# Kernel optimization log

Measured on AMD Instinct MI355X. Metric: run time of the kernel, lower is better.

The kernel has to match this reference:

```python
import jax, jax.numpy as jnp
import numpy as np

B, N, F = 512, 2048, 64
T = 4            # number of atom types
H1, H2 = 64, 32  # hidden widths; final layer outputs 1 (per-atom energy)


def setup_inputs() -> dict:
    key = jax.random.key(0)
    ks = jax.random.split(key, 8)
    x = jax.random.normal(ks[0], (B, N, F), dtype=jnp.float32)
    atomic_numbers = jax.random.randint(ks[1], (N,), 0, T)
    s = 0.05
    # Per-type MLP parameters, stacked over the type axis (torch Linear layout: [out, in]).
    w0 = jax.random.normal(ks[2], (T, H1, F), dtype=jnp.float32) * s
    b0 = jax.random.normal(ks[3], (T, H1), dtype=jnp.float32) * s
    w1 = jax.random.normal(ks[4], (T, H2, H1), dtype=jnp.float32) * s
    b1 = jax.random.normal(ks[5], (T, H2), dtype=jnp.float32) * s
    w2 = jax.random.normal(ks[6], (T, 1, H2), dtype=jnp.float32) * s
    b2 = jax.random.normal(ks[7], (T, 1), dtype=jnp.float32) * s
    return {"x": x, "atomic_numbers": atomic_numbers,
            "w0": w0, "b0": b0, "w1": w1, "b1": b1, "w2": w2, "b2": b2}


def reference(x, atomic_numbers, w0, b0, w1, b1, w2, b2):
    # Behler-Parrinello: route each atom through the MLP of its atom type,
    # then sum per-atom energies over atoms.  The torch version gathers atoms
    # by type, runs each type's MLP, and scatters back; here we evaluate all
    # T type-MLPs batched over the type axis and select with a one-hot mask
    # (identical math, jit-friendly, no data-dependent shapes).
    onehot = jax.nn.one_hot(atomic_numbers, w0.shape[0], dtype=x.dtype)  # [N, T]
    h = jax.nn.silu(jnp.einsum('bnf,thf->tbnh', x, w0) + b0[:, None, None, :])   # [T,B,N,H1]
    h = jax.nn.silu(jnp.einsum('tbnh,tgh->tbng', h, w1) + b1[:, None, None, :])  # [T,B,N,H2]
    e = jnp.einsum('tbng,tog->tbno', h, w2) + b2[:, None, None, :]               # [T,B,N,1]
    e = e[..., 0]                                                                # [T,B,N]
    per_atom = jnp.einsum('tbn,nt->bn', e, onehot)  # select the matching type per atom
    return per_atom.sum(axis=-1)                    # [B]
```

## Files before the change

### kernel.cpp

```cpp
#include <hip/hip_runtime.h>
#include <hip/hip_bf16.h>


#define B_ 512
#define N_ 2048
#define F_ 64
#define T_ 4
#define H1_ 64
#define H2_ 32

#define BT 16
#define NCHUNK 16

typedef __attribute__((ext_vector_type(8))) short bf16x8;
typedef __attribute__((ext_vector_type(4))) short bf16x4;
typedef __attribute__((ext_vector_type(4))) float f32x4;

__device__ inline float silu_f(float v) {
    return v * __builtin_amdgcn_rcpf(1.0f + __expf(-v));
}

__device__ inline bf16x8 pack8(float4 a, float4 b) {
    union { __hip_bfloat162 h[4]; bf16x8 v; } u;
    u.h[0] = __float22bfloat162_rn({a.x, a.y});
    u.h[1] = __float22bfloat162_rn({a.z, a.w});
    u.h[2] = __float22bfloat162_rn({b.x, b.y});
    u.h[3] = __float22bfloat162_rn({b.z, b.w});
    return u.v;
}

__device__ inline bf16x4 pack4(float a, float b, float c, float d) {
    union { __hip_bfloat162 h[2]; bf16x4 v; } u;
    u.h[0] = __float22bfloat162_rn({a, b});
    u.h[1] = __float22bfloat162_rn({c, d});
    return u.v;
}

__device__ inline float bf_at(bf16x4 v, int r) {
    union { bf16x4 v; __hip_bfloat16 h[4]; } u; u.v = v;
    return __bfloat162float(u.h[r]);
}

__global__ void sort_atoms(const int* __restrict__ an, int* __restrict__ sorted,
                           float* __restrict__ out) {
    const int lane = threadIdx.x;
#pragma unroll
    for (int i = 0; i < B_ / 64; ++i) out[i * 64 + lane] = 0.0f;

    int v[32];
#pragma unroll
    for (int c = 0; c < 32; ++c) v[c] = an[c * 64 + lane];

    int c0 = 0, c1 = 0, c2 = 0;
#pragma unroll
    for (int c = 0; c < 32; ++c) {
        c0 += __popcll(__ballot(v[c] == 0));
        c1 += __popcll(__ballot(v[c] == 1));
        c2 += __popcll(__ballot(v[c] == 2));
    }
    int base0 = 0, base1 = c0, base2 = c0 + c1, base3 = c0 + c1 + c2;
    const unsigned long long mb = (1ull << lane) - 1ull;
#pragma unroll
    for (int c = 0; c < 32; ++c) {
        const int t = v[c];
        unsigned long long m0 = __ballot(t == 0);
        unsigned long long m1 = __ballot(t == 1);
        unsigned long long m2 = __ballot(t == 2);
        unsigned long long m3 = __ballot(t == 3);
        int pos;
        if (t == 0)      pos = base0 + (int)__popcll(m0 & mb);
        else if (t == 1) pos = base1 + (int)__popcll(m1 & mb);
        else if (t == 2) pos = base2 + (int)__popcll(m2 & mb);
        else             pos = base3 + (int)__popcll(m3 & mb);
        sorted[pos] = (t << 16) | (c * 64 + lane);
        base0 += (int)__popcll(m0); base1 += (int)__popcll(m1);
        base2 += (int)__popcll(m2); base3 += (int)__popcll(m3);
    }
}

__global__ __launch_bounds__(64, 3) void bpnn_kernel(
    const float* __restrict__ x, const int* __restrict__ sorted,
    const float* __restrict__ w0, const float* __restrict__ b0,
    const float* __restrict__ w1, const float* __restrict__ b1,
    const float* __restrict__ w2, const float* __restrict__ b2,
    float* __restrict__ out)
{
    __shared__ __align__(16) __hip_bfloat16 trb[BT][68];

    const int lane = threadIdx.x;
    const int lr   = lane & 15;
    const int q    = lane >> 4;
    const int b0i  = blockIdx.y * BT;
    const int s0   = blockIdx.x * NCHUNK;

    int myid = 0;
    if (lane < NCHUNK) myid = sorted[s0 + lane];

    const float* xb_ = x + (size_t)(b0i + lr) * (N_ * F_) + q * 8;
    __hip_bfloat16* trbw = &trb[lr][0];

    float esum0 = 0.f, esum1 = 0.f, bsum = 0.f;

    bf16x8 aw000, aw001, aw010, aw011, aw020, aw021, aw030, aw031;
    bf16x8 aw100, aw101, aw110, aw111;
    bf16x4 b0f0, b0f1, b0f2, b0f3, b1f0, b1f1, w2f0, w2f1;
    float b2c = 0.f;

    int i = 0;
    int id0 = __builtin_amdgcn_readlane(myid, 0);
    int id1 = __builtin_amdgcn_readlane(myid, 1);
    float4 sa0, sa1, sa2, sa3, sb0, sb1, sb2, sb3;
    {
        const float4* pA = reinterpret_cast<const float4*>(xb_ + (size_t)(id0 & 0xFFFF) * F_);
        sa0 = pA[0]; sa1 = pA[1]; sa2 = pA[8]; sa3 = pA[9];
        const float4* pB = reinterpret_cast<const float4*>(xb_ + (size_t)(id1 & 0xFFFF) * F_);
        sb0 = pB[0]; sb1 = pB[1]; sb2 = pB[8]; sb3 = pB[9];
    }

    while (i < NCHUNK) {
        const int t = id0 >> 16;
        {
            const float* wb = w0 + t * (H1_ * F_) + lr * F_ + q * 8;
            const float4* pw;
            pw = reinterpret_cast<const float4*>(wb +  0 * F_ +  0); aw000 = pack8(pw[0], pw[1]);
            pw = reinterpret_cast<const float4*>(wb +  0 * F_ + 32); aw001 = pack8(pw[0], pw[1]);
            pw = reinterpret_cast<const float4*>(wb + 16 * F_ +  0); aw010 = pack8(pw[0], pw[1]);
            pw = reinterpret_cast<const float4*>(wb + 16 * F_ + 32); aw011 = pack8(pw[0], pw[1]);
            pw = reinterpret_cast<const float4*>(wb + 32 * F_ +  0); aw020 = pack8(pw[0], pw[1]);
            pw = reinterpret_cast<const float4*>(wb + 32 * F_ + 32); aw021 = pack8(pw[0], pw[1]);
            pw = reinterpret_cast<const float4*>(wb + 48 * F_ +  0); aw030 = pack8(pw[0], pw[1]);
            pw = reinterpret_cast<const float4*>(wb + 48 * F_ + 32); aw031 = pack8(pw[0], pw[1]);
            const float* wc = w1 + t * (H2_ * H1_) + lr * H1_ + q * 8;
            pw = reinterpret_cast<const float4*>(wc +  0 * H1_ +  0); aw100 = pack8(pw[0], pw[1]);
            pw = reinterpret_cast<const float4*>(wc +  0 * H1_ + 32); aw101 = pack8(pw[0], pw[1]);
            pw = reinterpret_cast<const float4*>(wc + 16 * H1_ +  0); aw110 = pack8(pw[0], pw[1]);
            pw = reinterpret_cast<const float4*>(wc + 16 * H1_ + 32); aw111 = pack8(pw[0], pw[1]);
            float4 v;
            v = *reinterpret_cast<const float4*>(b0 + t * H1_ +  0 + q * 4); b0f0 = pack4(v.x, v.y, v.z, v.w);
            v = *reinterpret_cast<const float4*>(b0 + t * H1_ + 16 + q * 4); b0f1 = pack4(v.x, v.y, v.z, v.w);
            v = *reinterpret_cast<const float4*>(b0 + t * H1_ + 32 + q * 4); b0f2 = pack4(v.x, v.y, v.z, v.w);
            v = *reinterpret_cast<const float4*>(b0 + t * H1_ + 48 + q * 4); b0f3 = pack4(v.x, v.y, v.z, v.w);
            v = *reinterpret_cast<const float4*>(b1 + t * H2_ +  0 + q * 4); b1f0 = pack4(v.x, v.y, v.z, v.w);
            v = *reinterpret_cast<const float4*>(b1 + t * H2_ + 16 + q * 4); b1f1 = pack4(v.x, v.y, v.z, v.w);
            v = *reinterpret_cast<const float4*>(w2 + t * H2_ +  0 + q * 4); w2f0 = pack4(v.x, v.y, v.z, v.w);
            v = *reinterpret_cast<const float4*>(w2 + t * H2_ + 16 + q * 4); w2f1 = pack4(v.x, v.y, v.z, v.w);
            b2c = b2[t];
        }

        for (;;) {
            bf16x8 xf0 = pack8(sa0, sa1);
            bf16x8 xf1 = pack8(sa2, sa3);
            sa0 = sb0; sa1 = sb1; sa2 = sb2; sa3 = sb3;
            int in2 = (i + 2 < NCHUNK) ? i + 2 : NCHUNK - 1;
            int idn = __builtin_amdgcn_readlane(myid, in2);
            {
                const float4* pB = reinterpret_cast<const float4*>(xb_ + (size_t)(idn & 0xFFFF) * F_);
                sb0 = pB[0]; sb1 = pB[1]; sb2 = pB[8]; sb3 = pB[9];
            }
            bsum += b2c;

            f32x4 acc0 = {0.f,0.f,0.f,0.f}, acc1 = {0.f,0.f,0.f,0.f};
            f32x4 acc2 = {0.f,0.f,0.f,0.f}, acc3 = {0.f,0.f,0.f,0.f};
            acc0 = __builtin_amdgcn_mfma_f32_16x16x32_bf16(aw000, xf0, acc0, 0, 0, 0);
            acc0 = __builtin_amdgcn_mfma_f32_16x16x32_bf16(aw001, xf1, acc0, 0, 0, 0);
            acc1 = __builtin_amdgcn_mfma_f32_16x16x32_bf16(aw010, xf0, acc1, 0, 0, 0);
            acc1 = __builtin_amdgcn_mfma_f32_16x16x32_bf16(aw011, xf1, acc1, 0, 0, 0);
            acc2 = __builtin_amdgcn_mfma_f32_16x16x32_bf16(aw020, xf0, acc2, 0, 0, 0);
            acc2 = __builtin_amdgcn_mfma_f32_16x16x32_bf16(aw021, xf1, acc2, 0, 0, 0);
            acc3 = __builtin_amdgcn_mfma_f32_16x16x32_bf16(aw030, xf0, acc3, 0, 0, 0);
            acc3 = __builtin_amdgcn_mfma_f32_16x16x32_bf16(aw031, xf1, acc3, 0, 0, 0);

            {
                float v0 = silu_f(acc0[0] + bf_at(b0f0, 0));
                float v1 = silu_f(acc0[1] + bf_at(b0f0, 1));
                float v2 = silu_f(acc0[2] + bf_at(b0f0, 2));
                float v3 = silu_f(acc0[3] + bf_at(b0f0, 3));
                *reinterpret_cast<bf16x4*>(trbw +  0 + q * 4) = pack4(v0, v1, v2, v3);
                v0 = silu_f(acc1[0] + bf_at(b0f1, 0));
                v1 = silu_f(acc1[1] + bf_at(b0f1, 1));
                v2 = silu_f(acc1[2] + bf_at(b0f1, 2));
                v3 = silu_f(acc1[3] + bf_at(b0f1, 3));
                *reinterpret_cast<bf16x4*>(trbw + 16 + q * 4) = pack4(v0, v1, v2, v3);
                v0 = silu_f(acc2[0] + bf_at(b0f2, 0));
                v1 = silu_f(acc2[1] + bf_at(b0f2, 1));
                v2 = silu_f(acc2[2] + bf_at(b0f2, 2));
                v3 = silu_f(acc2[3] + bf_at(b0f2, 3));
                *reinterpret_cast<bf16x4*>(trbw + 32 + q * 4) = pack4(v0, v1, v2, v3);
                v0 = silu_f(acc3[0] + bf_at(b0f3, 0));
                v1 = silu_f(acc3[1] + bf_at(b0f3, 1));
                v2 = silu_f(acc3[2] + bf_at(b0f3, 2));
                v3 = silu_f(acc3[3] + bf_at(b0f3, 3));
                *reinterpret_cast<bf16x4*>(trbw + 48 + q * 4) = pack4(v0, v1, v2, v3);
            }
            __builtin_amdgcn_wave_barrier();

            bf16x8 hb0 = *reinterpret_cast<const bf16x8*>(trbw + q * 8);
            bf16x8 hb1 = *reinterpret_cast<const bf16x8*>(trbw + 32 + q * 8);
            __builtin_amdgcn_wave_barrier();

            f32x4 acB0 = {0.f,0.f,0.f,0.f}, acB1 = {0.f,0.f,0.f,0.f};
            acB0 = __builtin_amdgcn_mfma_f32_16x16x32_bf16(aw100, hb0, acB0, 0, 0, 0);
            acB0 = __builtin_amdgcn_mfma_f32_16x16x32_bf16(aw101, hb1, acB0, 0, 0, 0);
            acB1 = __builtin_amdgcn_mfma_f32_16x16x32_bf16(aw110, hb0, acB1, 0, 0, 0);
            acB1 = __builtin_amdgcn_mfma_f32_16x16x32_bf16(aw111, hb1, acB1, 0, 0, 0);

#pragma unroll
            for (int r = 0; r < 4; ++r) {
                esum0 += silu_f(acB0[r] + bf_at(b1f0, r)) * bf_at(w2f0, r);
                esum1 += silu_f(acB1[r] + bf_at(b1f1, r)) * bf_at(w2f1, r);
            }

            ++i;
            id0 = id1; id1 = idn;
            if (i >= NCHUNK || (id0 >> 16) != t) break;
        }
    }

    float esum = esum0 + esum1;
    esum += __shfl_xor(esum, 16);
    esum += __shfl_xor(esum, 32);
    if (q == 0) atomicAdd(&out[b0i + lr], esum + bsum);
}

extern "C" void kernel_launch(void* const* d_in, const int* in_sizes, int n_in,
                              void* d_out, int out_size, void* d_ws, size_t ws_size,
                              hipStream_t stream) {
    const float* x  = (const float*)d_in[0];
    const int*   an = (const int*)d_in[1];
    const float* w0 = (const float*)d_in[2];
    const float* b0 = (const float*)d_in[3];
    const float* w1 = (const float*)d_in[4];
    const float* b1 = (const float*)d_in[5];
    const float* w2 = (const float*)d_in[6];
    const float* b2 = (const float*)d_in[7];
    float* out = (float*)d_out;
    int* sorted = (int*)d_ws;

    sort_atoms<<<1, 64, 0, stream>>>(an, sorted, out);
    dim3 grid(N_ / NCHUNK, B_ / BT);
    bpnn_kernel<<<grid, 64, 0, stream>>>(x, sorted, w0, b0, w1, b1, w2, b2, out);
}
```

Before: 393.1 us.

## Stage x rows via async global-to-LDS loads with 3-slot ring, 4-wave blocks

Replaces the register double-buffered x prefetch with `global_load_lds` async copies into a per-wave three-slot LDS ring. Manual `vmcnt` waits keep up to three atoms in flight. Blocks grow to four waves, each handling a 16-atom slice of a 64-atom chunk, which makes the grid four times smaller. The aim is to hide gather latency and cut register pressure, at the cost of extra LDS traffic and fragile hand-written waitcnt sequencing.

```diff
diff --git a/kernel.cpp b/kernel.cpp
--- a/kernel.cpp
+++ b/kernel.cpp
@@ -10,11 +10,17 @@
 #define H2_ 32
 
 #define BT 16
-#define NCHUNK 16
+#define WAVES 4
+#define NCHUNK 64
+#define WSLICE 16
+#define NSLOT 3
 
 typedef __attribute__((ext_vector_type(8))) short bf16x8;
 typedef __attribute__((ext_vector_type(4))) short bf16x4;
 typedef __attribute__((ext_vector_type(4))) float f32x4;
+
+typedef const __attribute__((address_space(1))) void* gas_ptr;
+typedef __attribute__((address_space(3))) void* las_ptr;
 
 __device__ inline float silu_f(float v) {
     return v * __builtin_amdgcn_rcpf(1.0f + __expf(-v));
@@ -78,26 +84,44 @@
     }
 }
 
-__global__ __launch_bounds__(64, 3) void bpnn_kernel(
+__global__ __launch_bounds__(256) void bpnn_kernel(
     const float* __restrict__ x, const int* __restrict__ sorted,
     const float* __restrict__ w0, const float* __restrict__ b0,
     const float* __restrict__ w1, const float* __restrict__ b1,
     const float* __restrict__ w2, const float* __restrict__ b2,
     float* __restrict__ out)
 {
-    __shared__ __align__(16) __hip_bfloat16 trb[BT][68];
-
-    const int lane = threadIdx.x;
+    __shared__ __align__(16) char xlds[WAVES][NSLOT][4096];
+    __shared__ __align__(16) __hip_bfloat16 trb[WAVES][BT][68];
+
+    const int tid  = threadIdx.x;
+    const int wave = tid >> 6;
+    const int lane = tid & 63;
     const int lr   = lane & 15;
     const int q    = lane >> 4;
     const int b0i  = blockIdx.y * BT;
-    const int s0   = blockIdx.x * NCHUNK;
-
-    int myid = 0;
-    if (lane < NCHUNK) myid = sorted[s0 + lane];
-
-    const float* xb_ = x + (size_t)(b0i + lr) * (N_ * F_) + q * 8;
-    __hip_bfloat16* trbw = &trb[lr][0];
+
+    const int myid = sorted[blockIdx.x * NCHUNK + lane];
+    const int w16  = wave * WSLICE;
+
+    const char* growbase = (const char*)x
+        + ((size_t)(b0i + lr) * (N_ * F_)) * sizeof(float) + (size_t)q * 16;
+    char* xw = &xlds[wave][0][0];
+    __hip_bfloat16* trbw = &trb[wave][lr][0];
+
+    auto stage = [&](int s, int n) {
+        const char* g = growbase + (size_t)n * 256;
+        char* l = xw + s * 4096;
+#pragma unroll
+        for (int c = 0; c < 4; ++c) {
+            __builtin_amdgcn_global_load_lds((gas_ptr)(g + c * 64),
+                                             (las_ptr)(l + c * 1024), 16, 0, 0);
+        }
+    };
+
+    stage(0, __builtin_amdgcn_readlane(myid, w16 + 0) & 0xFFFF);
+    stage(1, __builtin_amdgcn_readlane(myid, w16 + 1) & 0xFFFF);
+    stage(2, __builtin_amdgcn_readlane(myid, w16 + 2) & 0xFFFF);
 
     float esum0 = 0.f, esum1 = 0.f, bsum = 0.f;
 
@@ -105,21 +129,16 @@
     bf16x8 aw100, aw101, aw110, aw111;
     bf16x4 b0f0, b0f1, b0f2, b0f3, b1f0, b1f1, w2f0, w2f1;
     float b2c = 0.f;
-
-    int i = 0;
-    int id0 = __builtin_amdgcn_readlane(myid, 0);
-    int id1 = __builtin_amdgcn_readlane(myid, 1);
-    float4 sa0, sa1, sa2, sa3, sb0, sb1, sb2, sb3;
-    {
-        const float4* pA = reinterpret_cast<const float4*>(xb_ + (size_t)(id0 & 0xFFFF) * F_);
-        sa0 = pA[0]; sa1 = pA[1]; sa2 = pA[8]; sa3 = pA[9];
-        const float4* pB = reinterpret_cast<const float4*>(xb_ + (size_t)(id1 & 0xFFFF) * F_);
-        sb0 = pB[0]; sb1 = pB[1]; sb2 = pB[8]; sb3 = pB[9];
-    }
-
-    while (i < NCHUNK) {
-        const int t = id0 >> 16;
-        {
+    int cur_t = -1;
+    int slot = 0;
+
+    const char* rbase = xw + ((q >> 1) << 10) + ((q & 1) << 9) + (lr << 4);
+
+    for (int i = 0; i < WSLICE; ++i) {
+        const int id = __builtin_amdgcn_readlane(myid, w16 + i);
+        const int t  = id >> 16;
+        if (t != cur_t) {
+            cur_t = t;
             const float* wb = w0 + t * (H1_ * F_) + lr * F_ + q * 8;
             const float4* pw;
             pw = reinterpret_cast<const float4*>(wb +  0 * F_ +  0); aw000 = pack8(pw[0], pw[1]);
@@ -147,72 +166,77 @@
             b2c = b2[t];
         }
 
-        for (;;) {
-            bf16x8 xf0 = pack8(sa0, sa1);
-            bf16x8 xf1 = pack8(sa2, sa3);
-            sa0 = sb0; sa1 = sb1; sa2 = sb2; sa3 = sb3;
-            int in2 = (i + 2 < NCHUNK) ? i + 2 : NCHUNK - 1;
-            int idn = __builtin_amdgcn_readlane(myid, in2);
-            {
-                const float4* pB = reinterpret_cast<const float4*>(xb_ + (size_t)(idn & 0xFFFF) * F_);
-                sb0 = pB[0]; sb1 = pB[1]; sb2 = pB[8]; sb3 = pB[9];
-            }
-            bsum += b2c;
-
-            f32x4 acc0 = {0.f,0.f,0.f,0.f}, acc1 = {0.f,0.f,0.f,0.f};
-            f32x4 acc2 = {0.f,0.f,0.f,0.f}, acc3 = {0.f,0.f,0.f,0.f};
-            acc0 = __builtin_amdgcn_mfma_f32_16x16x32_bf16(aw000, xf0, acc0, 0, 0, 0);
-            acc0 = __builtin_amdgcn_mfma_f32_16x16x32_bf16(aw001, xf1, acc0, 0, 0, 0);
-            acc1 = __builtin_amdgcn_mfma_f32_16x16x32_bf16(aw010, xf0, acc1, 0, 0, 0);
-            acc1 = __builtin_amdgcn_mfma_f32_16x16x32_bf16(aw011, xf1, acc1, 0, 0, 0);
-            acc2 = __builtin_amdgcn_mfma_f32_16x16x32_bf16(aw020, xf0, acc2, 0, 0, 0);
-            acc2 = __builtin_amdgcn_mfma_f32_16x16x32_bf16(aw021, xf1, acc2, 0, 0, 0);
-            acc3 = __builtin_amdgcn_mfma_f32_16x16x32_bf16(aw030, xf0, acc3, 0, 0, 0);
-            acc3 = __builtin_amdgcn_mfma_f32_16x16x32_bf16(aw031, xf1, acc3, 0, 0, 0);
-
-            {
-                float v0 = silu_f(acc0[0] + bf_at(b0f0, 0));
-                float v1 = silu_f(acc0[1] + bf_at(b0f0, 1));
-                float v2 = silu_f(acc0[2] + bf_at(b0f0, 2));
-                float v3 = silu_f(acc0[3] + bf_at(b0f0, 3));
-                *reinterpret_cast<bf16x4*>(trbw +  0 + q * 4) = pack4(v0, v1, v2, v3);
-                v0 = silu_f(acc1[0] + bf_at(b0f1, 0));
-                v1 = silu_f(acc1[1] + bf_at(b0f1, 1));
-                v2 = silu_f(acc1[2] + bf_at(b0f1, 2));
-                v3 = silu_f(acc1[3] + bf_at(b0f1, 3));
-                *reinterpret_cast<bf16x4*>(trbw + 16 + q * 4) = pack4(v0, v1, v2, v3);
-                v0 = silu_f(acc2[0] + bf_at(b0f2, 0));
-                v1 = silu_f(acc2[1] + bf_at(b0f2, 1));
-                v2 = silu_f(acc2[2] + bf_at(b0f2, 2));
-                v3 = silu_f(acc2[3] + bf_at(b0f2, 3));
-                *reinterpret_cast<bf16x4*>(trbw + 32 + q * 4) = pack4(v0, v1, v2, v3);
-                v0 = silu_f(acc3[0] + bf_at(b0f3, 0));
-                v1 = silu_f(acc3[1] + bf_at(b0f3, 1));
-                v2 = silu_f(acc3[2] + bf_at(b0f3, 2));
-                v3 = silu_f(acc3[3] + bf_at(b0f3, 3));
-                *reinterpret_cast<bf16x4*>(trbw + 48 + q * 4) = pack4(v0, v1, v2, v3);
-            }
-            __builtin_amdgcn_wave_barrier();
-
-            bf16x8 hb0 = *reinterpret_cast<const bf16x8*>(trbw + q * 8);
-            bf16x8 hb1 = *reinterpret_cast<const bf16x8*>(trbw + 32 + q * 8);
-            __builtin_amdgcn_wave_barrier();
-
-            f32x4 acB0 = {0.f,0.f,0.f,0.f}, acB1 = {0.f,0.f,0.f,0.f};
-            acB0 = __builtin_amdgcn_mfma_f32_16x16x32_bf16(aw100, hb0, acB0, 0, 0, 0);
-            acB0 = __builtin_amdgcn_mfma_f32_16x16x32_bf16(aw101, hb1, acB0, 0, 0, 0);
-            acB1 = __builtin_amdgcn_mfma_f32_16x16x32_bf16(aw110, hb0, acB1, 0, 0, 0);
-            acB1 = __builtin_amdgcn_mfma_f32_16x16x32_bf16(aw111, hb1, acB1, 0, 0, 0);
-
-#pragma unroll
-            for (int r = 0; r < 4; ++r) {
-                esum0 += silu_f(acB0[r] + bf_at(b1f0, r)) * bf_at(w2f0, r);
-                esum1 += silu_f(acB1[r] + bf_at(b1f1, r)) * bf_at(w2f1, r);
-            }
-
-            ++i;
-            id0 = id1; id1 = idn;
-            if (i >= NCHUNK || (id0 >> 16) != t) break;
+        if (i < WSLICE - 2)      asm volatile("s_waitcnt vmcnt(8)" ::: "memory");
+        else if (i == WSLICE - 2) asm volatile("s_waitcnt vmcnt(4)" ::: "memory");
+        else                      asm volatile("s_waitcnt vmcnt(0)" ::: "memory");
+
+        const char* rb = rbase + slot * 4096;
+        float4 f0 = *reinterpret_cast<const float4*>(rb);
+        float4 f1 = *reinterpret_cast<const float4*>(rb + 256);
+        float4 f2 = *reinterpret_cast<const float4*>(rb + 2048);
+        float4 f3 = *reinterpret_cast<const float4*>(rb + 2304);
+        asm volatile("s_waitcnt lgkmcnt(0)" ::: "memory");
+        __builtin_amdgcn_sched_barrier(0);
+
+        if (i + NSLOT < WSLICE) {
+            int idn = __builtin_amdgcn_readlane(myid, w16 + i + NSLOT);
+            stage(slot, idn & 0xFFFF);
+        }
+        slot = (slot == NSLOT - 1) ? 0 : slot + 1;
+
+        bf16x8 xf0 = pack8(f0, f1);
+        bf16x8 xf1 = pack8(f2, f3);
+        bsum += b2c;
+
+        f32x4 acc0 = {0.f,0.f,0.f,0.f}, acc1 = {0.f,0.f,0.f,0.f};
+        f32x4 acc2 = {0.f,0.f,0.f,0.f}, acc3 = {0.f,0.f,0.f,0.f};
+        acc0 = __builtin_amdgcn_mfma_f32_16x16x32_bf16(aw000, xf0, acc0, 0, 0, 0);
+        acc0 = __builtin_amdgcn_mfma_f32_16x16x32_bf16(aw001, xf1, acc0, 0, 0, 0);
+        acc1 = __builtin_amdgcn_mfma_f32_16x16x32_bf16(aw010, xf0, acc1, 0, 0, 0);
+        acc1 = __builtin_amdgcn_mfma_f32_16x16x32_bf16(aw011, xf1, acc1, 0, 0, 0);
+        acc2 = __builtin_amdgcn_mfma_f32_16x16x32_bf16(aw020, xf0, acc2, 0, 0, 0);
+        acc2 = __builtin_amdgcn_mfma_f32_16x16x32_bf16(aw021, xf1, acc2, 0, 0, 0);
+        acc3 = __builtin_amdgcn_mfma_f32_16x16x32_bf16(aw030, xf0, acc3, 0, 0, 0);
+        acc3 = __builtin_amdgcn_mfma_f32_16x16x32_bf16(aw031, xf1, acc3, 0, 0, 0);
+
+        {
+            float v0 = silu_f(acc0[0] + bf_at(b0f0, 0));
+            float v1 = silu_f(acc0[1] + bf_at(b0f0, 1));
+            float v2 = silu_f(acc0[2] + bf_at(b0f0, 2));
+            float v3 = silu_f(acc0[3] + bf_at(b0f0, 3));
+            *reinterpret_cast<bf16x4*>(trbw +  0 + q * 4) = pack4(v0, v1, v2, v3);
+            v0 = silu_f(acc1[0] + bf_at(b0f1, 0));
+            v1 = silu_f(acc1[1] + bf_at(b0f1, 1));
+            v2 = silu_f(acc1[2] + bf_at(b0f1, 2));
+            v3 = silu_f(acc1[3] + bf_at(b0f1, 3));
+            *reinterpret_cast<bf16x4*>(trbw + 16 + q * 4) = pack4(v0, v1, v2, v3);
+            v0 = silu_f(acc2[0] + bf_at(b0f2, 0));
+            v1 = silu_f(acc2[1] + bf_at(b0f2, 1));
+            v2 = silu_f(acc2[2] + bf_at(b0f2, 2));
+            v3 = silu_f(acc2[3] + bf_at(b0f2, 3));
+            *reinterpret_cast<bf16x4*>(trbw + 32 + q * 4) = pack4(v0, v1, v2, v3);
+            v0 = silu_f(acc3[0] + bf_at(b0f3, 0));
+            v1 = silu_f(acc3[1] + bf_at(b0f3, 1));
+            v2 = silu_f(acc3[2] + bf_at(b0f3, 2));
+            v3 = silu_f(acc3[3] + bf_at(b0f3, 3));
+            *reinterpret_cast<bf16x4*>(trbw + 48 + q * 4) = pack4(v0, v1, v2, v3);
+        }
+        __builtin_amdgcn_wave_barrier();
+
+        bf16x8 hb0 = *reinterpret_cast<const bf16x8*>(trbw + q * 8);
+        bf16x8 hb1 = *reinterpret_cast<const bf16x8*>(trbw + 32 + q * 8);
+        __builtin_amdgcn_wave_barrier();
+
+        f32x4 acB0 = {0.f,0.f,0.f,0.f}, acB1 = {0.f,0.f,0.f,0.f};
+        acB0 = __builtin_amdgcn_mfma_f32_16x16x32_bf16(aw100, hb0, acB0, 0, 0, 0);
+        acB0 = __builtin_amdgcn_mfma_f32_16x16x32_bf16(aw101, hb1, acB0, 0, 0, 0);
+        acB1 = __builtin_amdgcn_mfma_f32_16x16x32_bf16(aw110, hb0, acB1, 0, 0, 0);
+        acB1 = __builtin_amdgcn_mfma_f32_16x16x32_bf16(aw111, hb1, acB1, 0, 0, 0);
+
+#pragma unroll
+        for (int r = 0; r < 4; ++r) {
+            esum0 += silu_f(acB0[r] + bf_at(b1f0, r)) * bf_at(w2f0, r);
+            esum1 += silu_f(acB1[r] + bf_at(b1f1, r)) * bf_at(w2f1, r);
         }
     }
 
@@ -238,5 +262,5 @@
 
     sort_atoms<<<1, 64, 0, stream>>>(an, sorted, out);
     dim3 grid(N_ / NCHUNK, B_ / BT);
-    bpnn_kernel<<<grid, 64, 0, stream>>>(x, sorted, w0, b0, w1, b1, w2, b2, out);
-}
+    bpnn_kernel<<<grid, 256, 0, stream>>>(x, sorted, w0, b0, w1, b1, w2, b2, out);
+}
```

After: 384.3 us. 1.02x faster.
